# Optimization experiments

Hardware: AMD Instinct MI355X
Metric: run time of the kernel (lower is better)

## Reference

```python
import jax, jax.numpy as jnp
import numpy as np

T, D, H, AE, DFF, B = 128, 256, 8, 32, 512, 256
EPS = 1e-5


def _xavier(key, shape):
    fan_in, fan_out = shape[-2], shape[-1]
    limit = float(np.sqrt(6.0 / (fan_in + fan_out)))
    return jax.random.uniform(key, shape, jnp.float32, -limit, limit)


def setup_inputs() -> dict:
    key = jax.random.key(0)
    ks = jax.random.split(key, 9)
    return {
        "X": jax.random.normal(ks[0], (B, T, D), jnp.float32),
        "Q": _xavier(ks[1], (T, D, H * AE)),
        "K": _xavier(ks[2], (T, D, H * AE)),
        "V": _xavier(ks[3], (T, D, H * D)),
        "O": _xavier(ks[4], (T, H * D, D)),
        "W_gate": _xavier(ks[5], (T, D, DFF)),
        "W_up": _xavier(ks[6], (T, D, DFF)),
        "W_down": _xavier(ks[7], (T, DFF, D)),
        "gamma1": jnp.ones((D,), jnp.float32),
        "beta1": jnp.zeros((D,), jnp.float32),
        "gamma2": jnp.ones((D,), jnp.float32),
        "beta2": jnp.zeros((D,), jnp.float32),
    }


def _layer_norm(x, gamma, beta):
    mu = jnp.mean(x, axis=-1, keepdims=True)
    var = jnp.mean((x - mu) ** 2, axis=-1, keepdims=True)
    return (x - mu) * jax.lax.rsqrt(var + EPS) * gamma + beta


def reference(X, Q, K, V, O, W_gate, W_up, W_down, gamma1, beta1, gamma2, beta2):
    b, t, d = X.shape
    # --- heterogeneous self-attention (dropout is identity in eval mode) ---
    q = jnp.einsum('btd,tde->bte', X, Q).reshape(b, t, H, AE)
    k = jnp.einsum('btd,tde->bte', X, K).reshape(b, t, H, AE)
    v = jnp.einsum('btd,tdn->btn', X, V).reshape(b, t, H, d)
    scores = jnp.einsum('bthe,bshe->bhts', q, k) / jnp.sqrt(jnp.float32(AE))
    attn = jax.nn.softmax(scores, axis=-1)
    out = jnp.einsum('bhts,bshd->bthd', attn, v).reshape(b, t, H * d)
    attn_out = jnp.einsum('btn,tnd->btd', out, O)
    x = _layer_norm(X + attn_out, gamma1, beta1)
    # --- token-specific SwishGLU FFN ---
    gate = jnp.einsum('btd,tdf->btf', x, W_gate)
    up = jnp.einsum('btd,tdf->btf', x, W_up)
    hidden = jax.nn.silu(gate) * up
    ffn_out = jnp.einsum('btf,tfd->btd', hidden, W_down)
    return _layer_norm(x + ffn_out, gamma2, beta2)
```

## Files before the change

### kernel.cpp

```cpp
#include <hip/hip_runtime.h>
#include <stdint.h>

#define DEVI static __device__ __forceinline__

typedef __attribute__((ext_vector_type(4))) float f32x4;
typedef __attribute__((ext_vector_type(8))) short bf8;
typedef __attribute__((ext_vector_type(4))) unsigned short u16x4;

DEVI unsigned short f2bf(float f) {
  unsigned u = __builtin_bit_cast(unsigned, f);
  u = (u + 0x7FFFu + ((u >> 16) & 1u)) >> 16;
  return (unsigned short)u;
}
DEVI float bf2f(unsigned short s) {
  return __builtin_bit_cast(float, ((unsigned)s) << 16);
}
DEVI unsigned cvt_pk_bf16(float lo, float hi) {
  unsigned r;
  asm("v_cvt_pk_bf16_f32 %0, %1, %2" : "=v"(r) : "v"(lo), "v"(hi));
  return r;
}
DEVI int swz(int row) { return (((row >> 2) ^ row) & 7) << 4; }
DEVI int swz32(int row) { return (((row >> 1) ^ row) & 3) << 4; }

DEVI void gload16(const void* g, void* l) {
  __builtin_amdgcn_global_load_lds(
      (const __attribute__((address_space(1))) unsigned*)g,
      (__attribute__((address_space(3))) unsigned*)l, 16, 0, 0);
}

template<bool OUT_BF16, int MI>
__global__ __launch_bounds__(512, 4)
void gemm_tk(const unsigned short* __restrict__ A, const float* __restrict__ W0,
             const float* __restrict__ W1, void* __restrict__ C,
             int Ka, int N, int lognx, int logmx, int ldC)
{
  const int j = blockIdx.x;
  const int t = (j & 7) + 8 * (j >> (3 + lognx + logmx));
  const int nblk = (j >> 3) & ((1 << lognx) - 1);
  const int mblk = (j >> (3 + lognx)) & ((1 << logmx) - 1);
  const int n0blk = nblk * 128;
  const float* Wsel = (n0blk >= N) ? W1 : W0;
  const int n0w = (n0blk >= N) ? (n0blk - N) : n0blk;

  const int tid = threadIdx.x;
  const int lane = tid & 63;
  const int wv = tid >> 6;
  const int wrow = wv * (MI * 16);

  __shared__ short As[2][MI * 128 * 32];
  __shared__ short Ws[2][128 * 32];

  f32x4 acc[MI][8];
#pragma unroll
  for (int i = 0; i < MI; ++i)
#pragma unroll
    for (int jj = 0; jj < 8; ++jj) acc[i][jj] = f32x4{0.f, 0.f, 0.f, 0.f};

  const long ldA = 128L * Ka;
  const unsigned short* Ab = A + (long)t * Ka + (long)mblk * 128 * ldA;
  const float* Wb = Wsel + (long)t * Ka * N + n0w;

  const int n0 = (tid & 31) * 4;
  const int kp = tid >> 5;

#pragma unroll
  for (int it = 0; it < MI; ++it) {
    int ci = tid + it * 512;
    int m = ci >> 2, cb = (ci & 3) * 16;
    gload16((const char*)(Ab + (long)m * ldA) + (cb ^ swz32(m)),
            (char*)(&As[0][0]) + ci * 16);
  }
  {
    f32x4 wlo = *(const f32x4*)(Wb + (long)(kp * 2) * N + n0);
    f32x4 whi = *(const f32x4*)(Wb + (long)(kp * 2 + 1) * N + n0);
#pragma unroll
    for (int jj = 0; jj < 4; ++jj) {
      int n = n0 + jj;
      *(unsigned*)((char*)(&Ws[0][0]) + n * 64 + ((kp * 4) ^ swz32(n))) =
          cvt_pk_bf16(wlo[jj], whi[jj]);
    }
  }

  const int nt = Ka >> 5;
  int cur = 0;
  for (int kt = 0; kt < nt; ++kt) {
    __syncthreads();
    const bool more = (kt + 1) < nt;
    f32x4 wlo, whi;
    if (more) {
      const unsigned short* An = Ab + (kt + 1) * 32;
#pragma unroll
      for (int it = 0; it < MI; ++it) {
        int ci = tid + it * 512;
        int m = ci >> 2, cb = (ci & 3) * 16;
        gload16((const char*)(An + (long)m * ldA) + (cb ^ swz32(m)),
                (char*)(&As[cur ^ 1][0]) + ci * 16);
      }
      const float* Wn = Wb + (long)(kt + 1) * 32 * N;
      wlo = *(const f32x4*)(Wn + (long)(kp * 2) * N + n0);
      whi = *(const f32x4*)(Wn + (long)(kp * 2 + 1) * N + n0);
    }
    const int kb2 = (lane >> 4) * 16;
    bf8 a[MI];
#pragma unroll
    for (int mi = 0; mi < MI; ++mi) {
      const int m0 = wrow + mi * 16 + (lane & 15);
      a[mi] = *(const bf8*)((const char*)(&As[cur][0]) + m0 * 64 + (kb2 ^ swz32(m0)));
    }
#pragma unroll
    for (int ni = 0; ni < 8; ++ni) {
      const int n = ni * 16 + (lane & 15);
      bf8 bfr = *(const bf8*)((const char*)(&Ws[cur][0]) + n * 64 + (kb2 ^ swz32(n)));
#pragma unroll
      for (int mi = 0; mi < MI; ++mi)
        acc[mi][ni] = __builtin_amdgcn_mfma_f32_16x16x32_bf16(a[mi], bfr, acc[mi][ni], 0, 0, 0);
    }
    if (more) {
#pragma unroll
      for (int jj = 0; jj < 4; ++jj) {
        int n = n0 + jj;
        *(unsigned*)((char*)(&Ws[cur ^ 1][0]) + n * 64 + ((kp * 4) ^ swz32(n))) =
            cvt_pk_bf16(wlo[jj], whi[jj]);
      }
    }
    cur ^= 1;
  }
#pragma unroll
  for (int mi = 0; mi < MI; ++mi)
#pragma unroll
    for (int ni = 0; ni < 8; ++ni)
#pragma unroll
      for (int r = 0; r < 4; ++r) {
        int m = mblk * 128 + wrow + mi * 16 + (lane >> 4) * 4 + r;
        int n = n0blk + ni * 16 + (lane & 15);
        long off = ((long)m * 128 + t) * ldC + n;
        float v = acc[mi][ni][r];
        if constexpr (OUT_BF16) reinterpret_cast<unsigned short*>(C)[off] = f2bf(v);
        else reinterpret_cast<float*>(C)[off] = v;
      }
}

__global__ __launch_bounds__(256)
void cvt_bf(const float* __restrict__ in, unsigned short* __restrict__ out, long n)
{
  long i = ((long)blockIdx.x * 256 + threadIdx.x) * 8;
  if (i >= n) return;
  f32x4 a = *reinterpret_cast<const f32x4*>(in + i);
  f32x4 b = *reinterpret_cast<const f32x4*>(in + i + 4);
  u16x4 w0, w1;
#pragma unroll
  for (int j = 0; j < 4; ++j) { w0[j] = f2bf(a[j]); w1[j] = f2bf(b[j]); }
  *reinterpret_cast<u16x4*>(out + i) = w0;
  *reinterpret_cast<u16x4*>(out + i + 4) = w1;
}

__global__ __launch_bounds__(256)
void trans_v(const unsigned short* __restrict__ vb, unsigned short* __restrict__ vT)
{
  const int bh = blockIdx.y;
  const int b = bh >> 3, h = bh & 7;
  const int tile = blockIdx.x;
  const int tt = tile >> 3;
  const int td = tile & 7;
  __shared__ unsigned short sm[32][33];
  const int rloc = threadIdx.x >> 3;
  const int q4 = (threadIdx.x & 7) * 4;
  {
    long off = ((long)b * 128 + tt * 32 + rloc) * 2048 + h * 256 + td * 32 + q4;
    u16x4 v = *reinterpret_cast<const u16x4*>(vb + off);
#pragma unroll
    for (int j = 0; j < 4; ++j) sm[rloc][q4 + j] = v[j];
  }
  __syncthreads();
  {
    u16x4 w;
#pragma unroll
    for (int j = 0; j < 4; ++j) w[j] = sm[q4 + j][rloc];
    long off = ((long)bh * 256 + td * 32 + rloc) * 128 + tt * 32 + q4;
    *reinterpret_cast<u16x4*>(vT + off) = w;
  }
}

__global__ __launch_bounds__(512, 4)
void attn_k(const unsigned short* __restrict__ qk, const unsigned short* __restrict__ vT,
            unsigned short* __restrict__ cat)
{
  const int h = blockIdx.x, b = blockIdx.y;
  const int tid = threadIdx.x, lane = tid & 63, wv = tid >> 6;
  const int wrow = wv * 16;

  __shared__ short ps[128 * 128];
  __shared__ short vs[2][256 * 32];

  const long qkBase = ((long)b * 128) * 512 + h * 32;
  const long vBase = ((long)(b * 8 + h)) * 256 * 128;
  const int kb_ = (lane >> 4) * 8;

#pragma unroll
  for (int it = 0; it < 2; ++it) {
    int ci = tid + it * 512;
    int d = ci >> 2, sc = ci & 3;
    gload16(vT + vBase + (long)d * 128 + (((sc * 16) ^ swz32(d)) >> 1),
            (char*)(&vs[0][0]) + ci * 16);
  }

  f32x4 sacc[8];
#pragma unroll
  for (int c = 0; c < 8; ++c) sacc[c] = f32x4{0.f, 0.f, 0.f, 0.f};
  bf8 aq;
  {
    int row = wrow + (lane & 15);
    aq = *reinterpret_cast<const bf8*>(qk + qkBase + (long)row * 512 + kb_);
  }
#pragma unroll
  for (int ni = 0; ni < 8; ++ni) {
    int s = ni * 16 + (lane & 15);
    bf8 bk = *reinterpret_cast<const bf8*>(qk + qkBase + 256 + (long)s * 512 + kb_);
    sacc[ni] = __builtin_amdgcn_mfma_f32_16x16x32_bf16(aq, bk, sacc[ni], 0, 0, 0);
  }

  const float scale = 0.17677669529663687f;
  float sinv[4];
#pragma unroll
  for (int r = 0; r < 4; ++r) {
    int row = wrow + (lane >> 4) * 4 + r;
    float vv[8];
    float mx = -1e30f;
#pragma unroll
    for (int c = 0; c < 8; ++c) { vv[c] = sacc[c][r] * scale; mx = fmaxf(mx, vv[c]); }
#pragma unroll
    for (int mm = 1; mm < 16; mm <<= 1) mx = fmaxf(mx, __shfl_xor(mx, mm, 64));
    float s_ = 0.f;
#pragma unroll
    for (int c = 0; c < 8; ++c) { vv[c] = __expf(vv[c] - mx); s_ += vv[c]; }
#pragma unroll
    for (int mm = 1; mm < 16; mm <<= 1) s_ += __shfl_xor(s_, mm, 64);
    sinv[r] = 1.0f / s_;
#pragma unroll
    for (int c = 0; c < 8; ++c) {
      int col = c * 16 + (lane & 15);
      int byte = row * 256 + ((col * 2) ^ swz(row));
      *reinterpret_cast<unsigned short*>(reinterpret_cast<char*>(ps) + byte) = f2bf(vv[c]);
    }
  }

  f32x4 oacc[16];
#pragma unroll
  for (int c = 0; c < 16; ++c) oacc[c] = f32x4{0.f, 0.f, 0.f, 0.f};

#pragma unroll 1
  for (int cs = 0; cs < 4; ++cs) {
    __syncthreads();
    if (cs < 3) {
#pragma unroll
      for (int it = 0; it < 2; ++it) {
        int ci = tid + it * 512;
        int d = ci >> 2, sc = ci & 3;
        gload16(vT + vBase + (long)d * 128 + (cs + 1) * 32 + (((sc * 16) ^ swz32(d)) >> 1),
                (char*)(&vs[(cs + 1) & 1][0]) + ci * 16);
      }
    }
    const int kglob = cs * 32 + kb_;
    bf8 ap;
    {
      int row = wrow + (lane & 15);
      int byte = row * 256 + ((kglob * 2) ^ swz(row));
      ap = *reinterpret_cast<const bf8*>(reinterpret_cast<const char*>(ps) + byte);
    }
    __builtin_amdgcn_s_setprio(1);
#pragma unroll
    for (int c = 0; c < 16; ++c) {
      int d = c * 16 + (lane & 15);
      bf8 bv = *reinterpret_cast<const bf8*>(
          reinterpret_cast<const char*>(&vs[cs & 1][0]) + d * 64 + ((kb_ * 2) ^ swz32(d)));
      oacc[c] = __builtin_amdgcn_mfma_f32_16x16x32_bf16(ap, bv, oacc[c], 0, 0, 0);
    }
    __builtin_amdgcn_s_setprio(0);
  }

#pragma unroll
  for (int c = 0; c < 16; ++c)
#pragma unroll
    for (int r = 0; r < 4; ++r) {
      int tt = wrow + (lane >> 4) * 4 + r;
      int d = c * 16 + (lane & 15);
      float v = oacc[c][r] * sinv[r];
      long off = ((long)b * 128 + tt) * 2048 + h * 256 + d;
      cat[off] = f2bf(v);
    }
}

template<bool WF, bool WB>
__global__ __launch_bounds__(256)
void ln_k(const unsigned short* __restrict__ a, const unsigned short* __restrict__ bsrc,
          const float* __restrict__ gamma, const float* __restrict__ beta,
          float* __restrict__ of, unsigned short* __restrict__ ob)
{
  const int row = blockIdx.x * 4 + (threadIdx.x >> 6);
  const int lane = threadIdx.x & 63;
  const long base = (long)row * 256 + lane * 4;
  u16x4 ua = *reinterpret_cast<const u16x4*>(a + base);
  u16x4 ub = *reinterpret_cast<const u16x4*>(bsrc + base);
  f32x4 x;
#pragma unroll
  for (int j = 0; j < 4; ++j) x[j] = bf2f(ua[j]) + bf2f(ub[j]);
  float s = x[0] + x[1] + x[2] + x[3];
  float s2 = x[0] * x[0] + x[1] * x[1] + x[2] * x[2] + x[3] * x[3];
#pragma unroll
  for (int mm = 1; mm < 64; mm <<= 1) { s += __shfl_xor(s, mm, 64); s2 += __shfl_xor(s2, mm, 64); }
  float mean = s * (1.f / 256.f);
  float var = fmaxf(s2 * (1.f / 256.f) - mean * mean, 0.f);
  float inv = rsqrtf(var + 1e-5f);
  f32x4 g = *reinterpret_cast<const f32x4*>(gamma + lane * 4);
  f32x4 be = *reinterpret_cast<const f32x4*>(beta + lane * 4);
  f32x4 y;
#pragma unroll
  for (int j = 0; j < 4; ++j) y[j] = (x[j] - mean) * inv * g[j] + be[j];
  if constexpr (WF) *reinterpret_cast<f32x4*>(of + base) = y;
  if constexpr (WB) {
    u16x4 w;
#pragma unroll
    for (int j = 0; j < 4; ++j) w[j] = f2bf(y[j]);
    *reinterpret_cast<u16x4*>(ob + base) = w;
  }
}

__global__ __launch_bounds__(256)
void silu_k(const unsigned short* __restrict__ gu, unsigned short* __restrict__ o, long n)
{
  long i = ((long)blockIdx.x * 256 + threadIdx.x) * 8;
  if (i >= n) return;
  long r = i >> 9;
  int f = (int)(i & 511);
  const unsigned short* g = gu + r * 1024 + f;
  const unsigned short* u = g + 512;
  u16x4 g0 = *reinterpret_cast<const u16x4*>(g);
  u16x4 g1 = *reinterpret_cast<const u16x4*>(g + 4);
  u16x4 u0 = *reinterpret_cast<const u16x4*>(u);
  u16x4 u1 = *reinterpret_cast<const u16x4*>(u + 4);
  u16x4 o0, o1;
#pragma unroll
  for (int j = 0; j < 4; ++j) {
    float gg = bf2f(g0[j]), uu = bf2f(u0[j]);
    o0[j] = f2bf(gg / (1.f + __expf(-gg)) * uu);
    gg = bf2f(g1[j]); uu = bf2f(u1[j]);
    o1[j] = f2bf(gg / (1.f + __expf(-gg)) * uu);
  }
  *reinterpret_cast<u16x4*>(o + i) = o0;
  *reinterpret_cast<u16x4*>(o + i + 4) = o1;
}

extern "C" void kernel_launch(void* const* d_in, const int* in_sizes, int n_in,
                              void* d_out, int out_size, void* d_ws, size_t ws_size,
                              hipStream_t stream)
{
  const float* X  = (const float*)d_in[0];
  const float* Qw = (const float*)d_in[1];
  const float* Kw = (const float*)d_in[2];
  const float* Vw = (const float*)d_in[3];
  const float* Ow = (const float*)d_in[4];
  const float* Wg = (const float*)d_in[5];
  const float* Wu = (const float*)d_in[6];
  const float* Wd = (const float*)d_in[7];
  const float* g1 = (const float*)d_in[8];
  const float* b1 = (const float*)d_in[9];
  const float* g2 = (const float*)d_in[10];
  const float* b2 = (const float*)d_in[11];

  char* ws = (char*)d_ws;
  const size_t MiB = 1048576;
  unsigned short* Xb  = (unsigned short*)(ws);
  unsigned short* qkb = (unsigned short*)(ws + 16 * MiB);
  char* regA = ws + 48 * MiB;
  char* regB = regA + 128 * MiB;

  unsigned short* vb     = (unsigned short*)regA;
  unsigned short* vT     = (unsigned short*)regB;
  unsigned short* cat    = (unsigned short*)regA;
  unsigned short* attnpb = (unsigned short*)(regB);
  unsigned short* x1b    = (unsigned short*)(regB + 16 * MiB);
  unsigned short* ffnb   = (unsigned short*)(regB + 32 * MiB);
  unsigned short* gateup = (unsigned short*)(regA);
  unsigned short* hidb   = (unsigned short*)(regA + 64 * MiB);
  float* out = (float*)d_out;

  dim3 blk(256), gblk(512);
  cvt_bf<<<dim3(4096), blk, 0, stream>>>(X, Xb, (long)8388608);
  gemm_tk<true, 2><<<dim3(512), gblk, 0, stream>>>(Xb, Qw, Kw, (void*)qkb, 256, 256, 2, 0, 512);
  gemm_tk<true, 2><<<dim3(2048), gblk, 0, stream>>>(Xb, Vw, Vw, (void*)vb, 256, 2048, 4, 0, 2048);
  trans_v<<<dim3(32, 2048), blk, 0, stream>>>(vb, vT);
  attn_k<<<dim3(8, 256), gblk, 0, stream>>>(qkb, vT, cat);
  gemm_tk<true, 1><<<dim3(512), gblk, 0, stream>>>(cat, Ow, Ow, (void*)attnpb, 2048, 256, 1, 1, 256);
  ln_k<false, true><<<dim3(8192), blk, 0, stream>>>(Xb, attnpb, g1, b1, (float*)nullptr, x1b);
  gemm_tk<true, 2><<<dim3(1024), gblk, 0, stream>>>(x1b, Wg, Wu, (void*)gateup, 256, 512, 3, 0, 1024);
  silu_k<<<dim3(8192), blk, 0, stream>>>(gateup, hidb, (long)16777216);
  gemm_tk<true, 1><<<dim3(512), gblk, 0, stream>>>(hidb, Wd, Wd, (void*)ffnb, 512, 256, 1, 1, 256);
  ln_k<true, false><<<dim3(8192), blk, 0, stream>>>(x1b, ffnb, g2, b2, out, (unsigned short*)nullptr);
}
```

Measured before the change: 535.2 us.

## Fuse V transpose into attention kernel via register-staged LDS transpose

Removes the separate trans_v kernel and has the attention kernel read V in its natural [b,t,h*d] layout. Each thread loads two consecutive token rows of 8 d-values into registers and writes them transposed, as packed pairs, into the swizzled LDS buffer. The V load is issued before the scores compute and before each chunk's MFMAs, with the LDS write placed after them, so the global load latency is hidden behind compute. This saves a full read and write of the 128 MiB V tensor plus one launch, at the cost of more scattered 4-byte LDS writes and extra registers in attn_k. The workspace layout is rearranged to match.

```diff
diff --git a/kernel.cpp b/kernel.cpp
--- a/kernel.cpp
+++ b/kernel.cpp
@@ -155,35 +155,22 @@
   *reinterpret_cast<u16x4*>(out + i + 4) = w1;
 }
 
-__global__ __launch_bounds__(256)
-void trans_v(const unsigned short* __restrict__ vb, unsigned short* __restrict__ vT)
-{
-  const int bh = blockIdx.y;
-  const int b = bh >> 3, h = bh & 7;
-  const int tile = blockIdx.x;
-  const int tt = tile >> 3;
-  const int td = tile & 7;
-  __shared__ unsigned short sm[32][33];
-  const int rloc = threadIdx.x >> 3;
-  const int q4 = (threadIdx.x & 7) * 4;
-  {
-    long off = ((long)b * 128 + tt * 32 + rloc) * 2048 + h * 256 + td * 32 + q4;
-    u16x4 v = *reinterpret_cast<const u16x4*>(vb + off);
-#pragma unroll
-    for (int j = 0; j < 4; ++j) sm[rloc][q4 + j] = v[j];
-  }
-  __syncthreads();
-  {
-    u16x4 w;
-#pragma unroll
-    for (int j = 0; j < 4; ++j) w[j] = sm[q4 + j][rloc];
-    long off = ((long)bh * 256 + td * 32 + rloc) * 128 + tt * 32 + q4;
-    *reinterpret_cast<u16x4*>(vT + off) = w;
+DEVI void stage_write_v(short* buf, f32x4 r0, f32x4 r1, int s2, int d0)
+{
+  const unsigned* a = reinterpret_cast<const unsigned*>(&r0);
+  const unsigned* c = reinterpret_cast<const unsigned*>(&r1);
+#pragma unroll
+  for (int j = 0; j < 8; ++j) {
+    unsigned lo = (j & 1) ? (a[j >> 1] >> 16) : (a[j >> 1] & 0xFFFFu);
+    unsigned hi = (j & 1) ? (c[j >> 1] >> 16) : (c[j >> 1] & 0xFFFFu);
+    int d = d0 + j;
+    *reinterpret_cast<unsigned*>(reinterpret_cast<char*>(buf) + d * 64 + ((4 * s2) ^ swz32(d))) =
+        lo | (hi << 16);
   }
 }
 
 __global__ __launch_bounds__(512, 4)
-void attn_k(const unsigned short* __restrict__ qk, const unsigned short* __restrict__ vT,
+void attn_k(const unsigned short* __restrict__ qk, const unsigned short* __restrict__ vg,
             unsigned short* __restrict__ cat)
 {
   const int h = blockIdx.x, b = blockIdx.y;
@@ -194,15 +181,17 @@
   __shared__ short vs[2][256 * 32];
 
   const long qkBase = ((long)b * 128) * 512 + h * 32;
-  const long vBase = ((long)(b * 8 + h)) * 256 * 128;
+  const long vgBase = ((long)b * 128) * 2048 + h * 256;
   const int kb_ = (lane >> 4) * 8;
 
-#pragma unroll
-  for (int it = 0; it < 2; ++it) {
-    int ci = tid + it * 512;
-    int d = ci >> 2, sc = ci & 3;
-    gload16(vT + vBase + (long)d * 128 + (((sc * 16) ^ swz32(d)) >> 1),
-            (char*)(&vs[0][0]) + ci * 16);
+  const int s2 = tid & 15;
+  const int d0 = (tid >> 4) * 8;
+
+  f32x4 r0, r1;
+  {
+    const unsigned short* src = vg + vgBase + (long)(2 * s2) * 2048 + d0;
+    r0 = *reinterpret_cast<const f32x4*>(src);
+    r1 = *reinterpret_cast<const f32x4*>(src + 2048);
   }
 
   f32x4 sacc[8];
@@ -245,6 +234,8 @@
     }
   }
 
+  stage_write_v(&vs[0][0], r0, r1, s2, d0);
+
   f32x4 oacc[16];
 #pragma unroll
   for (int c = 0; c < 16; ++c) oacc[c] = f32x4{0.f, 0.f, 0.f, 0.f};
@@ -253,13 +244,9 @@
   for (int cs = 0; cs < 4; ++cs) {
     __syncthreads();
     if (cs < 3) {
-#pragma unroll
-      for (int it = 0; it < 2; ++it) {
-        int ci = tid + it * 512;
-        int d = ci >> 2, sc = ci & 3;
-        gload16(vT + vBase + (long)d * 128 + (cs + 1) * 32 + (((sc * 16) ^ swz32(d)) >> 1),
-                (char*)(&vs[(cs + 1) & 1][0]) + ci * 16);
-      }
+      const unsigned short* src = vg + vgBase + (long)((cs + 1) * 32 + 2 * s2) * 2048 + d0;
+      r0 = *reinterpret_cast<const f32x4*>(src);
+      r1 = *reinterpret_cast<const f32x4*>(src + 2048);
     }
     const int kglob = cs * 32 + kb_;
     bf8 ap;
@@ -277,6 +264,7 @@
       oacc[c] = __builtin_amdgcn_mfma_f32_16x16x32_bf16(ap, bv, oacc[c], 0, 0, 0);
     }
     __builtin_amdgcn_s_setprio(0);
+    if (cs < 3) stage_write_v(&vs[(cs + 1) & 1][0], r0, r1, s2, d0);
   }
 
 #pragma unroll
@@ -376,21 +364,19 @@
   char* regB = regA + 128 * MiB;
 
   unsigned short* vb     = (unsigned short*)regA;
-  unsigned short* vT     = (unsigned short*)regB;
-  unsigned short* cat    = (unsigned short*)regA;
-  unsigned short* attnpb = (unsigned short*)(regB);
-  unsigned short* x1b    = (unsigned short*)(regB + 16 * MiB);
-  unsigned short* ffnb   = (unsigned short*)(regB + 32 * MiB);
-  unsigned short* gateup = (unsigned short*)(regA);
-  unsigned short* hidb   = (unsigned short*)(regA + 64 * MiB);
+  unsigned short* cat    = (unsigned short*)regB;
+  unsigned short* attnpb = (unsigned short*)(regA);
+  unsigned short* x1b    = (unsigned short*)(regA + 16 * MiB);
+  unsigned short* gateup = (unsigned short*)(regA + 32 * MiB);
+  unsigned short* hidb   = (unsigned short*)(regA + 96 * MiB);
+  unsigned short* ffnb   = (unsigned short*)(regA + 32 * MiB);
   float* out = (float*)d_out;
 
   dim3 blk(256), gblk(512);
   cvt_bf<<<dim3(4096), blk, 0, stream>>>(X, Xb, (long)8388608);
   gemm_tk<true, 2><<<dim3(512), gblk, 0, stream>>>(Xb, Qw, Kw, (void*)qkb, 256, 256, 2, 0, 512);
   gemm_tk<true, 2><<<dim3(2048), gblk, 0, stream>>>(Xb, Vw, Vw, (void*)vb, 256, 2048, 4, 0, 2048);
-  trans_v<<<dim3(32, 2048), blk, 0, stream>>>(vb, vT);
-  attn_k<<<dim3(8, 256), gblk, 0, stream>>>(qkb, vT, cat);
+  attn_k<<<dim3(8, 256), gblk, 0, stream>>>(qkb, vb, cat);
   gemm_tk<true, 1><<<dim3(512), gblk, 0, stream>>>(cat, Ow, Ow, (void*)attnpb, 2048, 256, 1, 1, 256);
   ln_k<false, true><<<dim3(8192), blk, 0, stream>>>(Xb, attnpb, g1, b1, (float*)nullptr, x1b);
   gemm_tk<true, 2><<<dim3(1024), gblk, 0, stream>>>(x1b, Wg, Wu, (void*)gateup, 256, 512, 3, 0, 1024);
```

New measurement: 465.1 us. -13.1%, faster.
